# Performance work log

Measured on AMD Instinct MI355X. Metric: run time of the kernel, lower is better.

Reference implementation:

```python
import jax, jax.numpy as jnp
import numpy as np

B, S, D = 64, 1024, 128
EPS = 1e-5

def hardswish(x):
    return x * jnp.clip(x + 3.0, 0.0, 6.0) / 6.0

def setup_inputs() -> dict:
    key = jax.random.key(0)
    k1, k2, k3 = jax.random.split(key, 3)
    x = jax.random.normal(k1, (B, S, D), dtype=jnp.float32)
    ln_w = jnp.ones((S, D), dtype=jnp.float32)
    ln_b = jnp.zeros((S, D), dtype=jnp.float32)
    # U1[i]/U2[i] rows packed into lower-triangular (S,S); init ~ N(0,1)*0.01
    W1 = jax.random.normal(k2, (S, S), dtype=jnp.float32) * 0.01
    W2 = jax.random.normal(k3, (S, S), dtype=jnp.float32) * 0.01
    return {"x": x, "ln_w": ln_w, "ln_b": ln_b, "W1": W1, "W2": W2}

def reference(x, ln_w, ln_b, W1, W2):
    # LayerNorm over the last two dims (seq_len, feature_dim) jointly
    mu = jnp.mean(x, axis=(-2, -1), keepdims=True)
    var = jnp.mean(jnp.square(x - mu), axis=(-2, -1), keepdims=True)
    h = (x - mu) * jax.lax.rsqrt(var + EPS) * ln_w + ln_b
    # causal (lower-triangular) time mixing: u[:, t] = sum_{s<=t} W1[t, s] * h[:, s]
    mask = jnp.tril(jnp.ones((S, S), dtype=x.dtype))
    u = hardswish(jnp.einsum('ts,bsd->btd', W1 * mask, h))
    v = jnp.einsum('ts,bsd->btd', W2 * mask, u)
    return x + v
```

## Files before the change

kernel.cpp:

```cpp
#include <hip/hip_runtime.h>
#include <hip/hip_bf16.h>

#define NB 64
#define S_ 1024
#define D_ 128

typedef __attribute__((ext_vector_type(8))) short bf16x8;
typedef __attribute__((ext_vector_type(4))) float f32x4;


__device__ __forceinline__ unsigned short f2bf(float f) {
  __hip_bfloat16 h = __float2bfloat16(f);
  return __builtin_bit_cast(unsigned short, h);
}

__device__ __forceinline__ void async_copy16(const void* g, void* l) {
  __builtin_amdgcn_global_load_lds(
      (const __attribute__((address_space(1))) unsigned int*)g,
      (__attribute__((address_space(3))) unsigned int*)l, 16, 0, 0);
}

__global__ __launch_bounds__(256) void prep_kernel(
    const float* __restrict__ x, const float* __restrict__ W1,
    const float* __restrict__ W2, float2* __restrict__ part,
    unsigned short* __restrict__ W1f, unsigned short* __restrict__ W2f) {
  const int blk = blockIdx.x;
  if (blk < 1024) {
    const int b = blk >> 4, c = blk & 15, t = threadIdx.x;
    const float4* xb = (const float4*)(x + (size_t)b * (S_ * D_) + c * 8192);
    float s = 0.f, q = 0.f;
#pragma unroll
    for (int i = 0; i < 8; ++i) {
      float4 v = xb[i * 256 + t];
      s += v.x + v.y + v.z + v.w;
      q += v.x * v.x + v.y * v.y + v.z * v.z + v.w * v.w;
    }
#pragma unroll
    for (int o = 32; o > 0; o >>= 1) {
      s += __shfl_down(s, o, 64);
      q += __shfl_down(q, o, 64);
    }
    __shared__ float2 w4[4];
    const int wave = t >> 6, lane = t & 63;
    if (lane == 0) w4[wave] = make_float2(s, q);
    __syncthreads();
    if (t == 0) {
      float ss = 0.f, qq = 0.f;
#pragma unroll
      for (int i = 0; i < 4; ++i) { ss += w4[i].x; qq += w4[i].y; }
      part[blk] = make_float2(ss, qq);
    }
  } else {
    const int id = (blk - 1024) * 256 + threadIdx.x;
    const int perW = (S_ * S_) / 4;
    const float* src = (id < perW) ? W1 : W2;
    unsigned short* dst = (id < perW) ? W1f : W2f;
    const int i4 = (id < perW) ? id : id - perW;
    const int flat = i4 * 4;
    const int trow = flat >> 10;
    const int scol = flat & 1023;
    float4 v = ((const float4*)src)[i4];
    ushort4 o;
    o.x = f2bf((scol + 0 <= trow) ? v.x : 0.f);
    o.y = f2bf((scol + 1 <= trow) ? v.y : 0.f);
    o.z = f2bf((scol + 2 <= trow) ? v.z : 0.f);
    o.w = f2bf((scol + 3 <= trow) ? v.w : 0.f);
    const size_t fa = ((size_t)(trow >> 4) * 32 + (scol >> 5)) * 512 +
                      ((scol >> 3) & 3) * 128 + (trow & 15) * 8 + (scol & 4);
    *(ushort4*)(dst + fa) = o;
  }
}

__global__ __launch_bounds__(256) void norm_t_kernel(const float* __restrict__ x,
                                                     const float* __restrict__ w,
                                                     const float* __restrict__ bb,
                                                     const float2* __restrict__ part,
                                                     unsigned short* __restrict__ hTf) {
  __shared__ unsigned short lds[64 * 132];
  const int blk = blockIdx.x;
  const int b = blk >> 4;
  const int s0 = (blk & 15) * 64;
  const int t = threadIdx.x;
  const int wave = t >> 6, lane = t & 63;
  const int quad = lane >> 4, l16 = lane & 15;
  float sum = 0.f, sumq = 0.f;
#pragma unroll
  for (int i = 0; i < 16; ++i) {
    float2 p = part[b * 16 + i];
    sum += p.x; sumq += p.y;
  }
  const float inv = 1.0f / (S_ * D_);
  const float mu = sum * inv;
  const float rs = rsqrtf(sumq * inv - mu * mu + 1e-5f);

  const float4* xb = (const float4*)(x + ((size_t)b * S_ + s0) * D_);
  const float4* wb = (const float4*)(w + (size_t)s0 * D_);
  const float4* bv4 = (const float4*)(bb + (size_t)s0 * D_);
#pragma unroll
  for (int r = 0; r < 8; ++r) {
    const int f = r * 256 + t;
    const int srow = f >> 5;
    const int c4 = f & 31;
    float4 xv = xb[f];
    float4 wv = wb[f];
    float4 bvv = bv4[f];
    ushort4 o;
    o.x = f2bf((xv.x - mu) * rs * wv.x + bvv.x);
    o.y = f2bf((xv.y - mu) * rs * wv.y + bvv.y);
    o.z = f2bf((xv.z - mu) * rs * wv.z + bvv.z);
    o.w = f2bf((xv.w - mu) * rs * wv.w + bvv.w);
    *(ushort4*)(lds + srow * 132 + c4 * 4) = o;
  }
  __syncthreads();
  unsigned short* outp = hTf + (size_t)b * (D_ * S_);
  const int cg0 = (blk & 15) * 2;
#pragma unroll
  for (int ff = 0; ff < 4; ++ff) {
    const int f = wave * 4 + ff;
    const int p = f >> 1, cl = f & 1;
    const int d = p * 16 + l16;
    const int sb = cl * 32 + quad * 8;
    bf16x8 v;
#pragma unroll
    for (int j = 0; j < 8; ++j)
      v[j] = (short)lds[(sb + j) * 132 + d];
    *(bf16x8*)(outp + ((size_t)p * 32 + cg0 + cl) * 512 + lane * 8) = v;
  }
}

template <bool HSWISH>
__global__ __launch_bounds__(256, 4) void gemm_causal(
    const unsigned short* __restrict__ Af, const unsigned short* __restrict__ Bf,
    unsigned short* __restrict__ Uf, const float* __restrict__ Xres,
    float* __restrict__ Out) {
  __shared__ __align__(16) unsigned short ldsA[16384];

  const int t = threadIdx.x;
  const int wave = t >> 6, lane = t & 63;
  const int quad = lane >> 4, l16 = lane & 15;

  const int bi = blockIdx.x;
  const int xcd = bi & 7;
  const int slot = bi >> 3;
  const int b = xcd * 8 + (slot & 7);
  const int j = slot >> 3;
  const int mt = (j < 8) ? j : (j ^ 3);
  const int row0 = mt * 64;

  const int cend = 2 * (mt + 1);
  const int npan = (cend + 7) >> 3;

  const unsigned short* Ab = Af + (size_t)mt * 4 * 32 * 512;
  const unsigned short* Bb = Bf + (size_t)b * (D_ * S_);

  f32x4 acc[4][2] = {};
  bf16x8 Bp[4][2];
#pragma unroll
  for (int g = 0; g < 4; ++g) {
    const int gg = (g < cend) ? g : 0;
#pragma unroll
    for (int jj = 0; jj < 2; ++jj)
      Bp[g][jj] = *(const bf16x8*)(Bb + ((size_t)(wave * 2 + jj) * 32 + gg) * 512 + lane * 8);
  }

  for (int p = 0; p < npan; ++p) {
    if (p) __syncthreads();
    const int rem = cend - p * 8;
#pragma unroll
    for (int jc = 0; jc < 8; ++jc) {
      const int flat16 = jc * 256 + t;
      const int iw = flat16 >> 9;
      const int cc = (flat16 >> 6) & 7;
      const int li = flat16 & 63;
      if (cc < rem)
        async_copy16(Ab + ((size_t)iw * 32 + p * 8 + cc) * 512 + li * 8,
                     ldsA + flat16 * 8);
    }
    __syncthreads();
#pragma unroll
    for (int c = 0; c < 8; ++c) {
      const int g = p * 8 + c;
      if (g < cend) {
        bf16x8 af[4];
#pragma unroll
        for (int i = 0; i < 4; ++i)
          af[i] = *(const bf16x8*)(ldsA + i * 4096 + c * 512 + lane * 8);
        __builtin_amdgcn_s_setprio(1);
#pragma unroll
        for (int i = 0; i < 4; ++i)
#pragma unroll
          for (int jj = 0; jj < 2; ++jj)
            acc[i][jj] = __builtin_amdgcn_mfma_f32_16x16x32_bf16(
                af[i], Bp[c & 3][jj], acc[i][jj], 0, 0, 0);
        __builtin_amdgcn_s_setprio(0);
        const int gn = (g + 4 < cend) ? (g + 4) : 0;
#pragma unroll
        for (int jj = 0; jj < 2; ++jj)
          Bp[c & 3][jj] = *(const bf16x8*)(
              Bb + ((size_t)(wave * 2 + jj) * 32 + gn) * 512 + lane * 8);
      }
    }
  }

  if (HSWISH) {
    __syncthreads();
    unsigned short* ldsT = ldsA;
#pragma unroll
    for (int i = 0; i < 4; ++i)
#pragma unroll
      for (int jj = 0; jj < 2; ++jj) {
        ushort4 pk;
        float v0 = acc[i][jj][0], v1 = acc[i][jj][1], v2 = acc[i][jj][2], v3 = acc[i][jj][3];
        pk.x = f2bf(v0 * fminf(fmaxf(v0 + 3.f, 0.f), 6.f) * (1.f / 6.f));
        pk.y = f2bf(v1 * fminf(fmaxf(v1 + 3.f, 0.f), 6.f) * (1.f / 6.f));
        pk.z = f2bf(v2 * fminf(fmaxf(v2 + 3.f, 0.f), 6.f) * (1.f / 6.f));
        pk.w = f2bf(v3 * fminf(fmaxf(v3 + 3.f, 0.f), 6.f) * (1.f / 6.f));
        const int n = wave * 32 + jj * 16 + l16;
        const int m0 = i * 16 + quad * 4;
        *(ushort4*)(ldsT + n * 72 + m0) = pk;
      }
    __syncthreads();
    unsigned short* gU = Uf + (size_t)b * (D_ * S_);
#pragma unroll
    for (int ff = 0; ff < 4; ++ff) {
      const int f = wave * 4 + ff;
      const int p2 = f >> 1, cl = f & 1;
      const int d = p2 * 16 + l16;
      const int tb = cl * 32 + quad * 8;
      bf16x8 v = *(const bf16x8*)(ldsT + d * 72 + tb);
      *(bf16x8*)(gU + ((size_t)p2 * 32 + mt * 2 + cl) * 512 + lane * 8) = v;
    }
  } else {
    float* gO = Out + (size_t)b * S_ * D_;
    const float* gX = Xres + (size_t)b * S_ * D_;
#pragma unroll
    for (int i = 0; i < 4; ++i) {
      const int mrow0 = row0 + i * 16 + quad * 4;
#pragma unroll
      for (int jj = 0; jj < 2; ++jj) {
        const int col = wave * 32 + jj * 16 + l16;
#pragma unroll
        for (int r = 0; r < 4; ++r) {
          const int addr = (mrow0 + r) * D_ + col;
          gO[addr] = gX[addr] + acc[i][jj][r];
        }
      }
    }
  }
}

extern "C" void kernel_launch(void* const* d_in, const int* in_sizes, int n_in,
                              void* d_out, int out_size, void* d_ws, size_t ws_size,
                              hipStream_t stream) {
  const float* x = (const float*)d_in[0];
  const float* ln_w = (const float*)d_in[1];
  const float* ln_b = (const float*)d_in[2];
  const float* W1 = (const float*)d_in[3];
  const float* W2 = (const float*)d_in[4];
  float* out = (float*)d_out;

  char* ws = (char*)d_ws;
  float2* part = (float2*)ws;
  unsigned short* W1f = (unsigned short*)(ws + 16384);
  unsigned short* W2f = W1f + (size_t)S_ * S_;
  unsigned short* hTf = W2f + (size_t)S_ * S_;
  unsigned short* uTf = hTf + (size_t)NB * D_ * S_;

  prep_kernel<<<3072, 256, 0, stream>>>(x, W1, W2, part, W1f, W2f);
  norm_t_kernel<<<NB * 16, 256, 0, stream>>>(x, ln_w, ln_b, part, hTf);
  gemm_causal<true><<<1024, 256, 0, stream>>>(W1f, hTf, uTf, nullptr, nullptr);
  gemm_causal<false><<<1024, 256, 0, stream>>>(W2f, uTf, nullptr, x, out);
}
```

Baseline: 135.1 us.

## Fuse prep, norm and both causal GEMMs into one persistent kernel with grid barriers

Replaces four separate kernel launches with a single 1024-block kernel that runs stats plus weight packing, normalization/transpose, and the two causal GEMM phases, separated by atomic-counter grid barriers. A tiny init kernel zeroes the counters. The aim is to remove inter-kernel launch gaps and tail drain between stages. It relies on all 1024 blocks being co-resident (4 per CU at 256 threads), and the spin barrier with a guard timeout risks deadlock or silent wrong results if residency does not hold.

```diff
diff --git a/kernel.cpp b/kernel.cpp
--- a/kernel.cpp
+++ b/kernel.cpp
@@ -20,121 +20,31 @@
       (__attribute__((address_space(3))) unsigned int*)l, 16, 0, 0);
 }
 
-__global__ __launch_bounds__(256) void prep_kernel(
-    const float* __restrict__ x, const float* __restrict__ W1,
-    const float* __restrict__ W2, float2* __restrict__ part,
-    unsigned short* __restrict__ W1f, unsigned short* __restrict__ W2f) {
-  const int blk = blockIdx.x;
-  if (blk < 1024) {
-    const int b = blk >> 4, c = blk & 15, t = threadIdx.x;
-    const float4* xb = (const float4*)(x + (size_t)b * (S_ * D_) + c * 8192);
-    float s = 0.f, q = 0.f;
-#pragma unroll
-    for (int i = 0; i < 8; ++i) {
-      float4 v = xb[i * 256 + t];
-      s += v.x + v.y + v.z + v.w;
-      q += v.x * v.x + v.y * v.y + v.z * v.z + v.w * v.w;
-    }
-#pragma unroll
-    for (int o = 32; o > 0; o >>= 1) {
-      s += __shfl_down(s, o, 64);
-      q += __shfl_down(q, o, 64);
-    }
-    __shared__ float2 w4[4];
-    const int wave = t >> 6, lane = t & 63;
-    if (lane == 0) w4[wave] = make_float2(s, q);
-    __syncthreads();
-    if (t == 0) {
-      float ss = 0.f, qq = 0.f;
-#pragma unroll
-      for (int i = 0; i < 4; ++i) { ss += w4[i].x; qq += w4[i].y; }
-      part[blk] = make_float2(ss, qq);
-    }
-  } else {
-    const int id = (blk - 1024) * 256 + threadIdx.x;
-    const int perW = (S_ * S_) / 4;
-    const float* src = (id < perW) ? W1 : W2;
-    unsigned short* dst = (id < perW) ? W1f : W2f;
-    const int i4 = (id < perW) ? id : id - perW;
-    const int flat = i4 * 4;
-    const int trow = flat >> 10;
-    const int scol = flat & 1023;
-    float4 v = ((const float4*)src)[i4];
-    ushort4 o;
-    o.x = f2bf((scol + 0 <= trow) ? v.x : 0.f);
-    o.y = f2bf((scol + 1 <= trow) ? v.y : 0.f);
-    o.z = f2bf((scol + 2 <= trow) ? v.z : 0.f);
-    o.w = f2bf((scol + 3 <= trow) ? v.w : 0.f);
-    const size_t fa = ((size_t)(trow >> 4) * 32 + (scol >> 5)) * 512 +
-                      ((scol >> 3) & 3) * 128 + (trow & 15) * 8 + (scol & 4);
-    *(ushort4*)(dst + fa) = o;
-  }
-}
-
-__global__ __launch_bounds__(256) void norm_t_kernel(const float* __restrict__ x,
-                                                     const float* __restrict__ w,
-                                                     const float* __restrict__ bb,
-                                                     const float2* __restrict__ part,
-                                                     unsigned short* __restrict__ hTf) {
-  __shared__ unsigned short lds[64 * 132];
-  const int blk = blockIdx.x;
-  const int b = blk >> 4;
-  const int s0 = (blk & 15) * 64;
-  const int t = threadIdx.x;
-  const int wave = t >> 6, lane = t & 63;
-  const int quad = lane >> 4, l16 = lane & 15;
-  float sum = 0.f, sumq = 0.f;
-#pragma unroll
-  for (int i = 0; i < 16; ++i) {
-    float2 p = part[b * 16 + i];
-    sum += p.x; sumq += p.y;
-  }
-  const float inv = 1.0f / (S_ * D_);
-  const float mu = sum * inv;
-  const float rs = rsqrtf(sumq * inv - mu * mu + 1e-5f);
-
-  const float4* xb = (const float4*)(x + ((size_t)b * S_ + s0) * D_);
-  const float4* wb = (const float4*)(w + (size_t)s0 * D_);
-  const float4* bv4 = (const float4*)(bb + (size_t)s0 * D_);
-#pragma unroll
-  for (int r = 0; r < 8; ++r) {
-    const int f = r * 256 + t;
-    const int srow = f >> 5;
-    const int c4 = f & 31;
-    float4 xv = xb[f];
-    float4 wv = wb[f];
-    float4 bvv = bv4[f];
-    ushort4 o;
-    o.x = f2bf((xv.x - mu) * rs * wv.x + bvv.x);
-    o.y = f2bf((xv.y - mu) * rs * wv.y + bvv.y);
-    o.z = f2bf((xv.z - mu) * rs * wv.z + bvv.z);
-    o.w = f2bf((xv.w - mu) * rs * wv.w + bvv.w);
-    *(ushort4*)(lds + srow * 132 + c4 * 4) = o;
-  }
+__device__ __forceinline__ void grid_bar(unsigned* ctr, unsigned target) {
   __syncthreads();
-  unsigned short* outp = hTf + (size_t)b * (D_ * S_);
-  const int cg0 = (blk & 15) * 2;
-#pragma unroll
-  for (int ff = 0; ff < 4; ++ff) {
-    const int f = wave * 4 + ff;
-    const int p = f >> 1, cl = f & 1;
-    const int d = p * 16 + l16;
-    const int sb = cl * 32 + quad * 8;
-    bf16x8 v;
-#pragma unroll
-    for (int j = 0; j < 8; ++j)
-      v[j] = (short)lds[(sb + j) * 132 + d];
-    *(bf16x8*)(outp + ((size_t)p * 32 + cg0 + cl) * 512 + lane * 8) = v;
-  }
+  if (threadIdx.x == 0) {
+    __hip_atomic_fetch_add(ctr, 1u, __ATOMIC_RELEASE, __HIP_MEMORY_SCOPE_AGENT);
+    int guard = 0;
+    while (__hip_atomic_load(ctr, __ATOMIC_RELAXED, __HIP_MEMORY_SCOPE_AGENT) <
+           target) {
+      __builtin_amdgcn_s_sleep(2);
+      if (++guard > 4000000) break;
+    }
+    (void)__hip_atomic_load(ctr, __ATOMIC_ACQUIRE, __HIP_MEMORY_SCOPE_AGENT);
+  }
+  __syncthreads();
+}
+
+__global__ __launch_bounds__(64) void init_ctrs(unsigned* __restrict__ c) {
+  if (threadIdx.x < 16) c[threadIdx.x * 32] = 0u;
 }
 
 template <bool HSWISH>
-__global__ __launch_bounds__(256, 4) void gemm_causal(
+__device__ __forceinline__ void gemm_phase(
+    unsigned short* ldsA,
     const unsigned short* __restrict__ Af, const unsigned short* __restrict__ Bf,
     unsigned short* __restrict__ Uf, const float* __restrict__ Xres,
     float* __restrict__ Out) {
-  __shared__ __align__(16) unsigned short ldsA[16384];
-
   const int t = threadIdx.x;
   const int wave = t >> 6, lane = t & 63;
   const int quad = lane >> 4, l16 = lane & 15;
@@ -249,6 +159,123 @@
   }
 }
 
+__global__ __launch_bounds__(256, 4) void fused_kernel(
+    const float* __restrict__ x, const float* __restrict__ ln_w,
+    const float* __restrict__ ln_b, const float* __restrict__ W1,
+    const float* __restrict__ W2, float2* __restrict__ part,
+    unsigned short* __restrict__ W1f, unsigned short* __restrict__ W2f,
+    unsigned short* __restrict__ hTf, unsigned short* __restrict__ uTf,
+    float* __restrict__ out, unsigned* __restrict__ ctrs) {
+  __shared__ __align__(16) unsigned short smem[16384];
+
+  const int blk = blockIdx.x;
+  const int t = threadIdx.x;
+  const int wave = t >> 6, lane = t & 63;
+  const int quad = lane >> 4, l16 = lane & 15;
+
+  {
+    const int b = blk >> 4, c = blk & 15;
+    const float4* xb = (const float4*)(x + (size_t)b * (S_ * D_) + c * 8192);
+    float s = 0.f, q = 0.f;
+#pragma unroll
+    for (int i = 0; i < 8; ++i) {
+      float4 v = xb[i * 256 + t];
+      s += v.x + v.y + v.z + v.w;
+      q += v.x * v.x + v.y * v.y + v.z * v.z + v.w * v.w;
+    }
+#pragma unroll
+    for (int o = 32; o > 0; o >>= 1) {
+      s += __shfl_down(s, o, 64);
+      q += __shfl_down(q, o, 64);
+    }
+    float2* w4 = (float2*)smem;
+    if (lane == 0) w4[wave] = make_float2(s, q);
+    __syncthreads();
+    if (t == 0) {
+      float ss = 0.f, qq = 0.f;
+#pragma unroll
+      for (int i = 0; i < 4; ++i) { ss += w4[i].x; qq += w4[i].y; }
+      part[blk] = make_float2(ss, qq);
+    }
+    const int perW = (S_ * S_) / 4;
+#pragma unroll
+    for (int rep = 0; rep < 2; ++rep) {
+      const int id = rep * perW + blk * 256 + t;
+      const float* src = (id < perW) ? W1 : W2;
+      unsigned short* dst = (id < perW) ? W1f : W2f;
+      const int i4 = (id < perW) ? id : id - perW;
+      const int flat = i4 * 4;
+      const int trow = flat >> 10;
+      const int scol = flat & 1023;
+      float4 v = ((const float4*)src)[i4];
+      ushort4 o;
+      o.x = f2bf((scol + 0 <= trow) ? v.x : 0.f);
+      o.y = f2bf((scol + 1 <= trow) ? v.y : 0.f);
+      o.z = f2bf((scol + 2 <= trow) ? v.z : 0.f);
+      o.w = f2bf((scol + 3 <= trow) ? v.w : 0.f);
+      const size_t fa = ((size_t)(trow >> 4) * 32 + (scol >> 5)) * 512 +
+                        ((scol >> 3) & 3) * 128 + (trow & 15) * 8 + (scol & 4);
+      *(ushort4*)(dst + fa) = o;
+    }
+  }
+  grid_bar(ctrs + 0 * 32, 1024);
+
+  {
+    unsigned short* lds = smem;
+    const int b = blk >> 4;
+    const int s0 = (blk & 15) * 64;
+    float sum = 0.f, sumq = 0.f;
+#pragma unroll
+    for (int i = 0; i < 16; ++i) {
+      float2 p = part[b * 16 + i];
+      sum += p.x; sumq += p.y;
+    }
+    const float inv = 1.0f / (S_ * D_);
+    const float mu = sum * inv;
+    const float rs = rsqrtf(sumq * inv - mu * mu + 1e-5f);
+
+    const float4* xb = (const float4*)(x + ((size_t)b * S_ + s0) * D_);
+    const float4* wb = (const float4*)(ln_w + (size_t)s0 * D_);
+    const float4* bv4 = (const float4*)(ln_b + (size_t)s0 * D_);
+#pragma unroll
+    for (int r = 0; r < 8; ++r) {
+      const int f = r * 256 + t;
+      const int srow = f >> 5;
+      const int c4 = f & 31;
+      float4 xv = xb[f];
+      float4 wv = wb[f];
+      float4 bvv = bv4[f];
+      ushort4 o;
+      o.x = f2bf((xv.x - mu) * rs * wv.x + bvv.x);
+      o.y = f2bf((xv.y - mu) * rs * wv.y + bvv.y);
+      o.z = f2bf((xv.z - mu) * rs * wv.z + bvv.z);
+      o.w = f2bf((xv.w - mu) * rs * wv.w + bvv.w);
+      *(ushort4*)(lds + srow * 132 + c4 * 4) = o;
+    }
+    __syncthreads();
+    unsigned short* outp = hTf + (size_t)b * (D_ * S_);
+    const int cg0 = (blk & 15) * 2;
+#pragma unroll
+    for (int ff = 0; ff < 4; ++ff) {
+      const int f = wave * 4 + ff;
+      const int p = f >> 1, cl = f & 1;
+      const int d = p * 16 + l16;
+      const int sb = cl * 32 + quad * 8;
+      bf16x8 v;
+#pragma unroll
+      for (int jj = 0; jj < 8; ++jj)
+        v[jj] = (short)lds[(sb + jj) * 132 + d];
+      *(bf16x8*)(outp + ((size_t)p * 32 + cg0 + cl) * 512 + lane * 8) = v;
+    }
+  }
+  grid_bar(ctrs + 1 * 32, 1024);
+
+  gemm_phase<true>(smem, W1f, hTf, uTf, nullptr, nullptr);
+  grid_bar(ctrs + 2 * 32, 1024);
+
+  gemm_phase<false>(smem, W2f, uTf, nullptr, x, out);
+}
+
 extern "C" void kernel_launch(void* const* d_in, const int* in_sizes, int n_in,
                               void* d_out, int out_size, void* d_ws, size_t ws_size,
                               hipStream_t stream) {
@@ -261,13 +288,13 @@
 
   char* ws = (char*)d_ws;
   float2* part = (float2*)ws;
+  unsigned* ctrs = (unsigned*)(ws + 12288);
   unsigned short* W1f = (unsigned short*)(ws + 16384);
   unsigned short* W2f = W1f + (size_t)S_ * S_;
   unsigned short* hTf = W2f + (size_t)S_ * S_;
   unsigned short* uTf = hTf + (size_t)NB * D_ * S_;
 
-  prep_kernel<<<3072, 256, 0, stream>>>(x, W1, W2, part, W1f, W2f);
-  norm_t_kernel<<<NB * 16, 256, 0, stream>>>(x, ln_w, ln_b, part, hTf);
-  gemm_causal<true><<<1024, 256, 0, stream>>>(W1f, hTf, uTf, nullptr, nullptr);
-  gemm_causal<false><<<1024, 256, 0, stream>>>(W2f, uTf, nullptr, x, out);
-}
+  init_ctrs<<<1, 64, 0, stream>>>(ctrs);
+  fused_kernel<<<1024, 256, 0, stream>>>(x, ln_w, ln_b, W1, W2, part, W1f, W2f,
+                                         hTf, uTf, out, ctrs);
+}
```

New measurement: 468.8 us. +246.9%, slower.

## Fuse stats, weight packing and normalization into one kernel with atomic grid sync

Applied to the files above, without the earlier changes.

Merges the statistics pass, the weight mask/convert/pack pass and the normalize-transpose pass into a single kernel. Per-batch sums are accumulated with device-scope atomics plus a counter, and each block spin-waits until all 16 blocks of its batch have contributed. A tiny init kernel zeroes the counters. This removes one launch and keeps the x tile hot between the stats and normalize phases. It risks deadlock if not all 16 blocks of a batch are co-resident, which the guard loop only bounds, and it uses relaxed atomics with no explicit fence.

```diff
diff --git a/kernel.cpp b/kernel.cpp
--- a/kernel.cpp
+++ b/kernel.cpp
@@ -20,82 +20,102 @@
       (__attribute__((address_space(3))) unsigned int*)l, 16, 0, 0);
 }
 
-__global__ __launch_bounds__(256) void prep_kernel(
-    const float* __restrict__ x, const float* __restrict__ W1,
-    const float* __restrict__ W2, float2* __restrict__ part,
-    unsigned short* __restrict__ W1f, unsigned short* __restrict__ W2f) {
-  const int blk = blockIdx.x;
-  if (blk < 1024) {
-    const int b = blk >> 4, c = blk & 15, t = threadIdx.x;
-    const float4* xb = (const float4*)(x + (size_t)b * (S_ * D_) + c * 8192);
-    float s = 0.f, q = 0.f;
-#pragma unroll
-    for (int i = 0; i < 8; ++i) {
-      float4 v = xb[i * 256 + t];
-      s += v.x + v.y + v.z + v.w;
-      q += v.x * v.x + v.y * v.y + v.z * v.z + v.w * v.w;
-    }
-#pragma unroll
-    for (int o = 32; o > 0; o >>= 1) {
-      s += __shfl_down(s, o, 64);
-      q += __shfl_down(q, o, 64);
-    }
-    __shared__ float2 w4[4];
-    const int wave = t >> 6, lane = t & 63;
-    if (lane == 0) w4[wave] = make_float2(s, q);
-    __syncthreads();
-    if (t == 0) {
-      float ss = 0.f, qq = 0.f;
-#pragma unroll
-      for (int i = 0; i < 4; ++i) { ss += w4[i].x; qq += w4[i].y; }
-      part[blk] = make_float2(ss, qq);
-    }
-  } else {
-    const int id = (blk - 1024) * 256 + threadIdx.x;
-    const int perW = (S_ * S_) / 4;
-    const float* src = (id < perW) ? W1 : W2;
-    unsigned short* dst = (id < perW) ? W1f : W2f;
-    const int i4 = (id < perW) ? id : id - perW;
-    const int flat = i4 * 4;
-    const int trow = flat >> 10;
-    const int scol = flat & 1023;
-    float4 v = ((const float4*)src)[i4];
-    ushort4 o;
-    o.x = f2bf((scol + 0 <= trow) ? v.x : 0.f);
-    o.y = f2bf((scol + 1 <= trow) ? v.y : 0.f);
-    o.z = f2bf((scol + 2 <= trow) ? v.z : 0.f);
-    o.w = f2bf((scol + 3 <= trow) ? v.w : 0.f);
-    const size_t fa = ((size_t)(trow >> 4) * 32 + (scol >> 5)) * 512 +
-                      ((scol >> 3) & 3) * 128 + (trow & 15) * 8 + (scol & 4);
-    *(ushort4*)(dst + fa) = o;
-  }
-}
-
-__global__ __launch_bounds__(256) void norm_t_kernel(const float* __restrict__ x,
-                                                     const float* __restrict__ w,
-                                                     const float* __restrict__ bb,
-                                                     const float2* __restrict__ part,
-                                                     unsigned short* __restrict__ hTf) {
-  __shared__ unsigned short lds[64 * 132];
+__global__ __launch_bounds__(256) void init_stats(unsigned* __restrict__ c) {
+#pragma unroll
+  for (int i = 0; i < 8; ++i) c[threadIdx.x + i * 256] = 0u;
+}
+
+__global__ __launch_bounds__(256) void prep_norm_kernel(
+    const float* __restrict__ x, const float* __restrict__ ln_w,
+    const float* __restrict__ ln_b, const float* __restrict__ W1,
+    const float* __restrict__ W2, float* __restrict__ stats,
+    unsigned short* __restrict__ W1f, unsigned short* __restrict__ W2f,
+    unsigned short* __restrict__ hTf) {
+  __shared__ __align__(16) unsigned short lds[64 * 132 + 32];
+  float2* w4 = (float2*)(lds + 64 * 132);
+  float* mr = (float*)(lds + 64 * 132 + 16);
+
   const int blk = blockIdx.x;
   const int b = blk >> 4;
   const int s0 = (blk & 15) * 64;
   const int t = threadIdx.x;
   const int wave = t >> 6, lane = t & 63;
   const int quad = lane >> 4, l16 = lane & 15;
-  float sum = 0.f, sumq = 0.f;
-#pragma unroll
-  for (int i = 0; i < 16; ++i) {
-    float2 p = part[b * 16 + i];
-    sum += p.x; sumq += p.y;
-  }
-  const float inv = 1.0f / (S_ * D_);
-  const float mu = sum * inv;
-  const float rs = rsqrtf(sumq * inv - mu * mu + 1e-5f);
+
+  float* sb = stats + (size_t)b * 32;
+  unsigned* cntp = (unsigned*)sb + 2;
 
   const float4* xb = (const float4*)(x + ((size_t)b * S_ + s0) * D_);
-  const float4* wb = (const float4*)(w + (size_t)s0 * D_);
-  const float4* bv4 = (const float4*)(bb + (size_t)s0 * D_);
+  {
+    float s = 0.f, q = 0.f;
+#pragma unroll
+    for (int i = 0; i < 8; ++i) {
+      float4 v = xb[i * 256 + t];
+      s += v.x + v.y + v.z + v.w;
+      q += v.x * v.x + v.y * v.y + v.z * v.z + v.w * v.w;
+    }
+#pragma unroll
+    for (int o = 32; o > 0; o >>= 1) {
+      s += __shfl_down(s, o, 64);
+      q += __shfl_down(q, o, 64);
+    }
+    if (lane == 0) w4[wave] = make_float2(s, q);
+  }
+  __syncthreads();
+  if (t == 0) {
+    float ss = 0.f, qq = 0.f;
+#pragma unroll
+    for (int i = 0; i < 4; ++i) { ss += w4[i].x; qq += w4[i].y; }
+    float o1 = __hip_atomic_fetch_add(sb + 0, ss, __ATOMIC_RELAXED,
+                                      __HIP_MEMORY_SCOPE_AGENT);
+    float o2 = __hip_atomic_fetch_add(sb + 1, qq, __ATOMIC_RELAXED,
+                                      __HIP_MEMORY_SCOPE_AGENT);
+    asm volatile("" ::"v"(o1), "v"(o2));
+    __hip_atomic_fetch_add(cntp, 1u, __ATOMIC_RELAXED,
+                           __HIP_MEMORY_SCOPE_AGENT);
+  }
+
+  {
+    const int u = blk * 4 + wave;
+    const int f = u & 2047;
+    const int p = f >> 5, c = f & 31;
+    const int r = p * 16 + l16;
+    const int k0 = c * 32 + quad * 8;
+    const float* wsrc = ((u >> 11) ? W2 : W1) + (size_t)r * 1024 + k0;
+    float4 a0 = ((const float4*)wsrc)[0];
+    float4 a1 = ((const float4*)wsrc)[1];
+    float av[8] = {a0.x, a0.y, a0.z, a0.w, a1.x, a1.y, a1.z, a1.w};
+    bf16x8 o;
+#pragma unroll
+    for (int jj = 0; jj < 8; ++jj)
+      o[jj] = (short)f2bf((k0 + jj <= r) ? av[jj] : 0.f);
+    unsigned short* dstp = ((u >> 11) ? W2f : W1f) +
+                           ((size_t)p * 32 + c) * 512 + lane * 8;
+    *(bf16x8*)dstp = o;
+  }
+
+  if (t == 0) {
+    int guard = 0;
+    while (__hip_atomic_load(cntp, __ATOMIC_RELAXED,
+                             __HIP_MEMORY_SCOPE_AGENT) < 16u) {
+      __builtin_amdgcn_s_sleep(4);
+      if (++guard > 400000) break;
+    }
+    float s1 = __hip_atomic_load(sb + 0, __ATOMIC_RELAXED,
+                                 __HIP_MEMORY_SCOPE_AGENT);
+    float s2 = __hip_atomic_load(sb + 1, __ATOMIC_RELAXED,
+                                 __HIP_MEMORY_SCOPE_AGENT);
+    const float inv = 1.0f / (S_ * D_);
+    const float mu = s1 * inv;
+    mr[0] = mu;
+    mr[1] = rsqrtf(s2 * inv - mu * mu + 1e-5f);
+  }
+  __syncthreads();
+  const float mu = mr[0];
+  const float rs = mr[1];
+
+  const float4* wb = (const float4*)(ln_w + (size_t)s0 * D_);
+  const float4* bv4 = (const float4*)(ln_b + (size_t)s0 * D_);
 #pragma unroll
   for (int r = 0; r < 8; ++r) {
     const int f = r * 256 + t;
@@ -119,11 +139,11 @@
     const int f = wave * 4 + ff;
     const int p = f >> 1, cl = f & 1;
     const int d = p * 16 + l16;
-    const int sb = cl * 32 + quad * 8;
+    const int sbase = cl * 32 + quad * 8;
     bf16x8 v;
 #pragma unroll
-    for (int j = 0; j < 8; ++j)
-      v[j] = (short)lds[(sb + j) * 132 + d];
+    for (int jj = 0; jj < 8; ++jj)
+      v[jj] = (short)lds[(sbase + jj) * 132 + d];
     *(bf16x8*)(outp + ((size_t)p * 32 + cg0 + cl) * 512 + lane * 8) = v;
   }
 }
@@ -260,14 +280,15 @@
   float* out = (float*)d_out;
 
   char* ws = (char*)d_ws;
-  float2* part = (float2*)ws;
+  float* stats = (float*)ws;
   unsigned short* W1f = (unsigned short*)(ws + 16384);
   unsigned short* W2f = W1f + (size_t)S_ * S_;
   unsigned short* hTf = W2f + (size_t)S_ * S_;
   unsigned short* uTf = hTf + (size_t)NB * D_ * S_;
 
-  prep_kernel<<<3072, 256, 0, stream>>>(x, W1, W2, part, W1f, W2f);
-  norm_t_kernel<<<NB * 16, 256, 0, stream>>>(x, ln_w, ln_b, part, hTf);
+  init_stats<<<1, 256, 0, stream>>>((unsigned*)stats);
+  prep_norm_kernel<<<1024, 256, 0, stream>>>(x, ln_w, ln_b, W1, W2, stats,
+                                             W1f, W2f, hTf);
   gemm_causal<true><<<1024, 256, 0, stream>>>(W1f, hTf, uTf, nullptr, nullptr);
   gemm_causal<false><<<1024, 256, 0, stream>>>(W2f, uTf, nullptr, x, out);
 }
```

Result: no change. 133.4 us (-1.3%).
